# Kernel tuning notes

Measured on AMD Instinct MI355X. Metric: run time of the kernel, lower is better.

Reference implementation:

```python
import jax, jax.numpy as jnp
import numpy as np

N, E = 50000, 800000
IN, HID, OUT = 256, 128, 128


def setup_inputs() -> dict:
    key = jax.random.key(0)
    ks = jax.random.split(key, 6)
    x = jax.random.normal(ks[0], (N, IN), dtype=jnp.float32)
    edge_index = jax.random.randint(ks[1], (2, E), 0, N, dtype=jnp.int32)
    # xavier_normal-ish scales (exact init values irrelevant for correctness baseline)
    W1 = jax.random.normal(ks[2], (IN, HID), dtype=jnp.float32) * (1.414 / np.sqrt(IN))
    att_src = jax.random.normal(ks[3], (HID,), dtype=jnp.float32) * 0.1
    att_dst = jax.random.normal(ks[4], (HID,), dtype=jnp.float32) * 0.1
    W2 = jax.random.normal(ks[5], (HID, OUT), dtype=jnp.float32) * (1.414 / np.sqrt(HID))
    return {"x": x, "edge_index": edge_index, "W1": W1,
            "att_src": att_src, "att_dst": att_dst, "W2": W2}


def _gat_layer(x, edge_index, W, a_src, a_dst):
    """GATConv(heads=1, concat=False, add_self_loops=False, dropout=0), attention=True."""
    n = x.shape[0]
    src, dst = edge_index[0], edge_index[1]  # message x_j = h[src], grouped by index = dst
    h = x @ W                                 # (N, C)
    e_src = h @ a_src                         # (N,) per-node attention logits
    e_dst = h @ a_dst                         # (N,)
    # per-edge: sigmoid(alpha_j + alpha_i), then scatter-softmax over dst neighborhoods
    alpha = jax.nn.sigmoid(e_src[src] + e_dst[dst])             # (E,)
    m = jax.ops.segment_max(alpha, dst, num_segments=n)          # stable softmax max
    ex = jnp.exp(alpha - m[dst])
    denom = jax.ops.segment_sum(ex, dst, num_segments=n)
    w = ex / denom[dst]                                          # (E,)
    # scatter-add aggregation of weighted source features; heads=1 so mean over heads is identity
    return jax.ops.segment_sum(h[src] * w[:, None], dst, num_segments=n)  # (N, C)


def reference(x, edge_index, W1, att_src, att_dst, W2):
    h1 = jax.nn.elu(_gat_layer(x, edge_index, W1, att_src, att_dst))
    # conv2 called with attention=False: mm(h1, W2).view(N,1,C).mean(1) == plain linear
    return h1 @ W2
```

## Files before the change

kernel.cpp:

```cpp
#include <hip/hip_runtime.h>
#include <hip/hip_bf16.h>

#define N_NODES 50000
#define N_EDGES 800000
#define DIN 256
#define DHID 128
#define DOUT 128
#define NBUCK 196
#define BINBLK 256
#define EPB 3125
#define BINIT 13

typedef __attribute__((ext_vector_type(8))) short bf16x8;
typedef __attribute__((ext_vector_type(4))) float f32x4;

__device__ inline unsigned short f2b(float f) {
    __hip_bfloat16 b = __float2bfloat16(f);
    return *reinterpret_cast<unsigned short*>(&b);
}

__global__ __launch_bounds__(256) void convW_kernel(
    const float* __restrict__ W1, const float* __restrict__ W2,
    unsigned short* __restrict__ W1t, unsigned short* __restrict__ W2t)
{
    int i = blockIdx.x * 256 + threadIdx.x;
    if (i < DIN * DHID) {
        int n = i >> 8, k = i & 255;
        W1t[i] = f2b(W1[k * DHID + n]);
    } else {
        int j = i - DIN * DHID;
        int n = j >> 7, k = j & 127;
        W2t[j] = f2b(W2[k * DOUT + n]);
    }
}

__global__ __launch_bounds__(256) void gemm1_mfma(
    const float* __restrict__ x,
    const unsigned short* __restrict__ W1t,
    const float* __restrict__ att_src,
    const float* __restrict__ att_dst,
    unsigned short* __restrict__ hb,
    float* __restrict__ es,
    float* __restrict__ ed)
{
    __shared__ unsigned short W1s[DHID * DIN];

    const int tid = threadIdx.x;
    const int wave = tid >> 6, lane = tid & 63;
    const int row0 = blockIdx.x * 64 + wave * 16;
    const int m = lane & 15, q = lane >> 4;

    {
        const float4* src = (const float4*)W1t;
        float4* dst = (float4*)W1s;
        #pragma unroll
        for (int i = 0; i < 16; ++i)
            dst[tid + i * 256] = src[tid + i * 256];
    }
    __syncthreads();

    int r  = row0 + m;
    int rc = (r < N_NODES) ? r : 0;

    f32x4 acc[8];
    #pragma unroll
    for (int t = 0; t < 8; ++t) acc[t] = (f32x4){0.f, 0.f, 0.f, 0.f};

    const float* xr = x + (size_t)rc * DIN + q * 8;
    const short* wp = (const short*)W1s + q * 8;

    #pragma unroll
    for (int kt = 0; kt < 8; ++kt) {
        float4 f0 = *(const float4*)(xr + kt * 32);
        float4 f1 = *(const float4*)(xr + kt * 32 + 4);
        bf16x8 a;
        a[0] = (short)f2b(f0.x); a[1] = (short)f2b(f0.y);
        a[2] = (short)f2b(f0.z); a[3] = (short)f2b(f0.w);
        a[4] = (short)f2b(f1.x); a[5] = (short)f2b(f1.y);
        a[6] = (short)f2b(f1.z); a[7] = (short)f2b(f1.w);
        #pragma unroll
        for (int t = 0; t < 8; ++t) {
            bf16x8 b = *(const bf16x8*)(wp + (t * 16 + m) * DIN + kt * 32);
            acc[t] = __builtin_amdgcn_mfma_f32_16x16x32_bf16(a, b, acc[t], 0, 0, 0);
        }
    }

    #pragma unroll
    for (int reg = 0; reg < 4; ++reg) {
        int rr = row0 + q * 4 + reg;
        if (rr < N_NODES) {
            #pragma unroll
            for (int t = 0; t < 8; ++t)
                hb[(size_t)rr * DHID + t * 16 + m] = f2b(acc[t][reg]);
        }
    }

    float esr[4] = {0.f, 0.f, 0.f, 0.f}, edr[4] = {0.f, 0.f, 0.f, 0.f};
    #pragma unroll
    for (int t = 0; t < 8; ++t) {
        float as = att_src[t * 16 + m];
        float ad = att_dst[t * 16 + m];
        #pragma unroll
        for (int reg = 0; reg < 4; ++reg) {
            esr[reg] += acc[t][reg] * as;
            edr[reg] += acc[t][reg] * ad;
        }
    }
    #pragma unroll
    for (int off = 8; off; off >>= 1)
        #pragma unroll
        for (int reg = 0; reg < 4; ++reg) {
            esr[reg] += __shfl_xor(esr[reg], off);
            edr[reg] += __shfl_xor(edr[reg], off);
        }
    if (m == 0) {
        #pragma unroll
        for (int reg = 0; reg < 4; ++reg) {
            int rr = row0 + q * 4 + reg;
            if (rr < N_NODES) { es[rr] = esr[reg]; ed[rr] = edr[reg]; }
        }
    }
}

__global__ __launch_bounds__(256) void lhist_kernel(
    const int* __restrict__ ei, int* __restrict__ blockHist,
    int* __restrict__ bucketTotals)
{
    __shared__ int h[NBUCK];
    const int t = threadIdx.x, blk = blockIdx.x;
    if (t < NBUCK) h[t] = 0;
    __syncthreads();
    const int base = blk * EPB;
    #pragma unroll 1
    for (int it = 0; it < BINIT; ++it) {
        int e = base + it * 256 + t;
        if (e < base + EPB)
            atomicAdd(&h[ei[N_EDGES + e] >> 8], 1);
    }
    __syncthreads();
    if (t < NBUCK) {
        blockHist[t * 256 + blk] = h[t];
        atomicAdd(&bucketTotals[t], h[t]);
    }
}

__global__ __launch_bounds__(256) void scanfused_kernel(
    const int* __restrict__ bucketTotals,
    const int* __restrict__ blockHist,
    int* __restrict__ matrixScan)
{
    __shared__ int bs[256];
    __shared__ int s[256];
    const int t = threadIdx.x, b = blockIdx.x;

    bs[t] = (t < NBUCK) ? bucketTotals[t] : 0;
    __syncthreads();
    #pragma unroll
    for (int off = 1; off < 256; off <<= 1) {
        int u = (t >= off) ? bs[t - off] : 0;
        __syncthreads();
        bs[t] += u;
        __syncthreads();
    }
    const int base = (b == 0) ? 0 : bs[b - 1];

    int c = blockHist[b * 256 + t];
    s[t] = c;
    __syncthreads();
    #pragma unroll
    for (int off = 1; off < 256; off <<= 1) {
        int u = (t >= off) ? s[t - off] : 0;
        __syncthreads();
        s[t] += u;
        __syncthreads();
    }
    matrixScan[b * 256 + t] = base + s[t] - c;
}

__global__ __launch_bounds__(256) void binpass_kernel(
    const int* __restrict__ ei,
    const float* __restrict__ es,
    const float* __restrict__ ed,
    const int* __restrict__ matrixScan,
    int2* __restrict__ binned)
{
    __shared__ int lcur[NBUCK];
    const int t = threadIdx.x, blk = blockIdx.x;
    if (t < NBUCK) lcur[t] = matrixScan[t * 256 + blk];
    __syncthreads();
    const int base = blk * EPB;
    #pragma unroll 1
    for (int it = 0; it < BINIT; ++it) {
        int e = base + it * 256 + t;
        if (e < base + EPB) {
            int s = ei[e];
            int d = ei[N_EDGES + e];
            float a  = es[s] + ed[d];
            float sg = 1.f / (1.f + __expf(-a));
            float w  = __expf(sg);
            int pos = atomicAdd(&lcur[d >> 8], 1);
            binned[pos] = make_int2(s | ((d & 255) << 16), __float_as_int(w));
        }
    }
}

__global__ __launch_bounds__(256) void sortpass_kernel(
    const int2* __restrict__ binned,
    const int* __restrict__ matrixScan,
    int2* __restrict__ sortedSW,
    int* __restrict__ offset,
    int* __restrict__ count)
{
    __shared__ int lhist[256], lscan[256], lcur[256];
    const int t = threadIdx.x, b = blockIdx.x;
    const int start = matrixScan[b * 256];
    const int end   = (b == NBUCK - 1) ? N_EDGES : matrixScan[(b + 1) * 256];
    const int cnt   = end - start;

    lhist[t] = 0;
    __syncthreads();
    for (int i = t; i < cnt; i += 256)
        atomicAdd(&lhist[(binned[start + i].x >> 16) & 255], 1);
    __syncthreads();

    int v = lhist[t];
    lscan[t] = v;
    __syncthreads();
    #pragma unroll
    for (int off = 1; off < 256; off <<= 1) {
        int u = (t >= off) ? lscan[t - off] : 0;
        __syncthreads();
        lscan[t] += u;
        __syncthreads();
    }
    int excl = lscan[t] - v;

    int node = (b << 8) + t;
    if (node < N_NODES) { offset[node] = start + excl; count[node] = v; }
    lcur[t] = excl;
    __syncthreads();

    for (int i = t; i < cnt; i += 256) {
        int2 ent = binned[start + i];
        int dlow = (ent.x >> 16) & 255;
        int pos = atomicAdd(&lcur[dlow], 1);
        sortedSW[start + pos] = make_int2(ent.x & 0xFFFF, ent.y);
    }
}

__global__ __launch_bounds__(256) void agg_kernel(
    const int2* __restrict__ sortedSW,
    const int* __restrict__ offset,
    const int* __restrict__ count,
    const unsigned short* __restrict__ hb,
    unsigned int* __restrict__ h1b)
{
    int node = (blockIdx.x * 256 + threadIdx.x) >> 6;
    int lane = threadIdx.x & 63;
    if (node >= N_NODES) return;

    int beg = offset[node];
    int deg = count[node];

    float2 acc = make_float2(0.f, 0.f);
    float wsum = 0.f;

    for (int base = 0; base < deg; base += 64) {
        int cnt = min(64, deg - base);
        int2 sw = (lane < cnt) ? sortedSW[beg + base + lane] : make_int2(0, 0);
        int j = 0;

#define TIER(T)                                                                 \
        for (; j + T <= cnt; j += T) {                                          \
            unsigned uu[T]; float ww[T];                                        \
            _Pragma("unroll")                                                   \
            for (int k = 0; k < T; ++k) {                                       \
                int s_ = __builtin_amdgcn_readlane(sw.x, j + k);                \
                uu[k] = *(const unsigned*)(hb + (size_t)s_ * DHID + 2 * lane);  \
            }                                                                   \
            _Pragma("unroll")                                                   \
            for (int k = 0; k < T; ++k)                                         \
                ww[k] = __uint_as_float(                                        \
                    (unsigned)__builtin_amdgcn_readlane(sw.y, j + k));          \
            _Pragma("unroll")                                                   \
            for (int k = 0; k < T; ++k) {                                       \
                wsum  += ww[k];                                                 \
                acc.x += ww[k] * __uint_as_float(uu[k] << 16);                  \
                acc.y += ww[k] * __uint_as_float(uu[k] & 0xffff0000u);          \
            }                                                                   \
        }

        TIER(16)
        TIER(8)
        TIER(4)
#undef TIER
        for (; j < cnt; ++j) {
            int   sj = __builtin_amdgcn_readlane(sw.x, j);
            float wj = __uint_as_float((unsigned)__builtin_amdgcn_readlane(sw.y, j));
            unsigned u = *(const unsigned*)(hb + (size_t)sj * DHID + 2 * lane);
            acc.x += wj * __uint_as_float(u << 16);
            acc.y += wj * __uint_as_float(u & 0xffff0000u);
            wsum  += wj;
        }
    }
    float inv = (deg > 0) ? 1.f / wsum : 0.f;
    float v0 = acc.x * inv, v1 = acc.y * inv;
    float e0 = v0 > 0.f ? v0 : (__expf(v0) - 1.f);
    float e1 = v1 > 0.f ? v1 : (__expf(v1) - 1.f);
    h1b[(size_t)node * (DHID / 2) + lane] =
        (unsigned)f2b(e0) | ((unsigned)f2b(e1) << 16);
}

__global__ __launch_bounds__(256) void gemm2_mfma(
    const unsigned short* __restrict__ h1b,
    const unsigned short* __restrict__ W2t,
    float* __restrict__ out)
{
    __shared__ unsigned short W2s[DOUT * DHID];

    const int tid = threadIdx.x;
    const int wave = tid >> 6, lane = tid & 63;
    const int row0 = blockIdx.x * 64 + wave * 16;
    const int m = lane & 15, q = lane >> 4;

    {
        const float4* src = (const float4*)W2t;
        float4* dst = (float4*)W2s;
        #pragma unroll
        for (int i = 0; i < 8; ++i)
            dst[tid + i * 256] = src[tid + i * 256];
    }
    __syncthreads();

    int r  = row0 + m;
    int rc = (r < N_NODES) ? r : 0;

    f32x4 acc[8];
    #pragma unroll
    for (int t = 0; t < 8; ++t) acc[t] = (f32x4){0.f, 0.f, 0.f, 0.f};

    const short* xp = (const short*)h1b + (size_t)rc * DHID + q * 8;
    const short* wp = (const short*)W2s + q * 8;

    #pragma unroll
    for (int kt = 0; kt < 4; ++kt) {
        bf16x8 a = *(const bf16x8*)(xp + kt * 32);
        #pragma unroll
        for (int t = 0; t < 8; ++t) {
            bf16x8 b = *(const bf16x8*)(wp + (t * 16 + m) * DHID + kt * 32);
            acc[t] = __builtin_amdgcn_mfma_f32_16x16x32_bf16(a, b, acc[t], 0, 0, 0);
        }
    }

    #pragma unroll
    for (int reg = 0; reg < 4; ++reg) {
        int rr = row0 + q * 4 + reg;
        if (rr < N_NODES) {
            #pragma unroll
            for (int t = 0; t < 8; ++t)
                out[(size_t)rr * DOUT + t * 16 + m] = acc[t][reg];
        }
    }
}

extern "C" void kernel_launch(void* const* d_in, const int* in_sizes, int n_in,
                              void* d_out, int out_size, void* d_ws, size_t ws_size,
                              hipStream_t stream)
{
    const float* x    = (const float*)d_in[0];
    const int*   ei   = (const int*)d_in[1];
    const float* W1   = (const float*)d_in[2];
    const float* asrc = (const float*)d_in[3];
    const float* adst = (const float*)d_in[4];
    const float* W2   = (const float*)d_in[5];
    float*       out  = (float*)d_out;

    char* p = (char*)d_ws;
    unsigned short* hb  = (unsigned short*)p;  p += (size_t)N_NODES * DHID * 2;
    unsigned int*   h1b = (unsigned int*)p;    p += (size_t)N_NODES * DHID * 2;
    unsigned short* W1t = (unsigned short*)p;  p += (size_t)DHID * DIN * 2;
    unsigned short* W2t = (unsigned short*)p;  p += (size_t)DOUT * DHID * 2;
    float* es     = (float*)p;  p += (size_t)N_NODES * 4;
    float* ed     = (float*)p;  p += (size_t)N_NODES * 4;
    int*   offset = (int*)p;    p += (size_t)N_NODES * 4;
    int*   count  = (int*)p;    p += (size_t)N_NODES * 4;
    int*   blockHist    = (int*)p; p += (size_t)NBUCK * 256 * 4;
    int*   matrixScan   = (int*)p; p += (size_t)NBUCK * 256 * 4;
    int*   bucketTotals = (int*)p; p += 256 * 4;
    int2*  binned   = (int2*)p; p += (size_t)N_EDGES * 8;
    int2*  sortedSW = (int2*)p; p += (size_t)N_EDGES * 8;

    hipMemsetAsync(bucketTotals, 0, NBUCK * sizeof(int), stream);

    convW_kernel<<<(DIN * DHID + DHID * DOUT) / 256, 256, 0, stream>>>(W1, W2, W1t, W2t);

    gemm1_mfma<<<(N_NODES + 63) / 64, 256, 0, stream>>>(x, W1t, asrc, adst, hb, es, ed);

    lhist_kernel    <<<BINBLK, 256, 0, stream>>>(ei, blockHist, bucketTotals);
    scanfused_kernel<<<NBUCK, 256, 0, stream>>>(bucketTotals, blockHist, matrixScan);
    binpass_kernel  <<<BINBLK, 256, 0, stream>>>(ei, es, ed, matrixScan, binned);
    sortpass_kernel <<<NBUCK, 256, 0, stream>>>(binned, matrixScan, sortedSW, offset, count);

    agg_kernel<<<(N_NODES * 64 + 255) / 256, 256, 0, stream>>>(
        sortedSW, offset, count, hb, h1b);

    gemm2_mfma<<<(N_NODES + 63) / 64, 256, 0, stream>>>((const unsigned short*)h1b, W2t, out);
}
```

Before: 195.2 us.

## Switch GEMMs to single-wave 32x32x16 MFMA blocks reading weights from global

Both dense GEMMs now use one-wave blocks of 32 rows with the 32x32x16 bf16 MFMA instead of four-wave blocks of 64 rows with 16x16x32 MFMA. The shared-memory staging of the transposed weight matrix and its barrier are removed, so B fragments are loaded straight from global memory and rely on L2/L1 caching. This is meant to cut the per-block LDS fill cost (64KB for W1) and raise occupancy, at the cost of more blocks and repeated global weight reads.

```diff
diff --git a/kernel.cpp b/kernel.cpp
--- a/kernel.cpp
+++ b/kernel.cpp
@@ -12,7 +12,7 @@
 #define BINIT 13
 
 typedef __attribute__((ext_vector_type(8))) short bf16x8;
-typedef __attribute__((ext_vector_type(4))) float f32x4;
+typedef __attribute__((ext_vector_type(16))) float f32x16;
 
 __device__ inline unsigned short f2b(float f) {
     __hip_bfloat16 b = __float2bfloat16(f);
@@ -34,7 +34,7 @@
     }
 }
 
-__global__ __launch_bounds__(256) void gemm1_mfma(
+__global__ __launch_bounds__(64) void gemm1_mfma(
     const float* __restrict__ x,
     const unsigned short* __restrict__ W1t,
     const float* __restrict__ att_src,
@@ -43,81 +43,74 @@
     float* __restrict__ es,
     float* __restrict__ ed)
 {
-    __shared__ unsigned short W1s[DHID * DIN];
-
-    const int tid = threadIdx.x;
-    const int wave = tid >> 6, lane = tid & 63;
-    const int row0 = blockIdx.x * 64 + wave * 16;
-    const int m = lane & 15, q = lane >> 4;
-
-    {
-        const float4* src = (const float4*)W1t;
-        float4* dst = (float4*)W1s;
-        #pragma unroll
-        for (int i = 0; i < 16; ++i)
-            dst[tid + i * 256] = src[tid + i * 256];
-    }
-    __syncthreads();
-
-    int r  = row0 + m;
+    const int lane = threadIdx.x;
+    const int row0 = blockIdx.x * 32;
+    const int c  = lane & 31;
+    const int hf = lane >> 5;
+
+    int r  = row0 + c;
     int rc = (r < N_NODES) ? r : 0;
 
-    f32x4 acc[8];
-    #pragma unroll
-    for (int t = 0; t < 8; ++t) acc[t] = (f32x4){0.f, 0.f, 0.f, 0.f};
-
-    const float* xr = x + (size_t)rc * DIN + q * 8;
-    const short* wp = (const short*)W1s + q * 8;
-
-    #pragma unroll
-    for (int kt = 0; kt < 8; ++kt) {
-        float4 f0 = *(const float4*)(xr + kt * 32);
-        float4 f1 = *(const float4*)(xr + kt * 32 + 4);
+    f32x16 acc[4];
+    #pragma unroll
+    for (int t = 0; t < 4; ++t)
+        #pragma unroll
+        for (int g = 0; g < 16; ++g) acc[t][g] = 0.f;
+
+    const float* xr = x + (size_t)rc * DIN + hf * 8;
+    const unsigned short* wb = W1t + hf * 8;
+
+    #pragma unroll
+    for (int kt = 0; kt < 16; ++kt) {
+        float4 f0 = *(const float4*)(xr + kt * 16);
+        float4 f1 = *(const float4*)(xr + kt * 16 + 4);
         bf16x8 a;
         a[0] = (short)f2b(f0.x); a[1] = (short)f2b(f0.y);
         a[2] = (short)f2b(f0.z); a[3] = (short)f2b(f0.w);
         a[4] = (short)f2b(f1.x); a[5] = (short)f2b(f1.y);
         a[6] = (short)f2b(f1.z); a[7] = (short)f2b(f1.w);
         #pragma unroll
-        for (int t = 0; t < 8; ++t) {
-            bf16x8 b = *(const bf16x8*)(wp + (t * 16 + m) * DIN + kt * 32);
-            acc[t] = __builtin_amdgcn_mfma_f32_16x16x32_bf16(a, b, acc[t], 0, 0, 0);
-        }
-    }
-
-    #pragma unroll
-    for (int reg = 0; reg < 4; ++reg) {
-        int rr = row0 + q * 4 + reg;
-        if (rr < N_NODES) {
+        for (int t = 0; t < 4; ++t) {
+            bf16x8 b = *(const bf16x8*)(wb + (size_t)(t * 32 + c) * DIN + kt * 16);
+            acc[t] = __builtin_amdgcn_mfma_f32_32x32x16_bf16(a, b, acc[t], 0, 0, 0);
+        }
+    }
+
+    #pragma unroll
+    for (int reg = 0; reg < 16; ++reg) {
+        int row = row0 + (reg & 3) + 4 * hf + 8 * (reg >> 2);
+        if (row < N_NODES) {
             #pragma unroll
-            for (int t = 0; t < 8; ++t)
-                hb[(size_t)rr * DHID + t * 16 + m] = f2b(acc[t][reg]);
-        }
-    }
-
-    float esr[4] = {0.f, 0.f, 0.f, 0.f}, edr[4] = {0.f, 0.f, 0.f, 0.f};
-    #pragma unroll
-    for (int t = 0; t < 8; ++t) {
-        float as = att_src[t * 16 + m];
-        float ad = att_dst[t * 16 + m];
-        #pragma unroll
-        for (int reg = 0; reg < 4; ++reg) {
+            for (int t = 0; t < 4; ++t)
+                hb[(size_t)row * DHID + t * 32 + c] = f2b(acc[t][reg]);
+        }
+    }
+
+    float esr[16], edr[16];
+    #pragma unroll
+    for (int reg = 0; reg < 16; ++reg) { esr[reg] = 0.f; edr[reg] = 0.f; }
+    #pragma unroll
+    for (int t = 0; t < 4; ++t) {
+        float as = att_src[t * 32 + c];
+        float ad = att_dst[t * 32 + c];
+        #pragma unroll
+        for (int reg = 0; reg < 16; ++reg) {
             esr[reg] += acc[t][reg] * as;
             edr[reg] += acc[t][reg] * ad;
         }
     }
     #pragma unroll
-    for (int off = 8; off; off >>= 1)
-        #pragma unroll
-        for (int reg = 0; reg < 4; ++reg) {
+    for (int off = 16; off; off >>= 1)
+        #pragma unroll
+        for (int reg = 0; reg < 16; ++reg) {
             esr[reg] += __shfl_xor(esr[reg], off);
             edr[reg] += __shfl_xor(edr[reg], off);
         }
-    if (m == 0) {
-        #pragma unroll
-        for (int reg = 0; reg < 4; ++reg) {
-            int rr = row0 + q * 4 + reg;
-            if (rr < N_NODES) { es[rr] = esr[reg]; ed[rr] = edr[reg]; }
+    if (c == 0) {
+        #pragma unroll
+        for (int reg = 0; reg < 16; ++reg) {
+            int row = row0 + (reg & 3) + 4 * hf + 8 * (reg >> 2);
+            if (row < N_NODES) { es[row] = esr[reg]; ed[row] = edr[reg]; }
         }
     }
 }
@@ -311,54 +304,45 @@
         (unsigned)f2b(e0) | ((unsigned)f2b(e1) << 16);
 }
 
-__global__ __launch_bounds__(256) void gemm2_mfma(
+__global__ __launch_bounds__(64) void gemm2_mfma(
     const unsigned short* __restrict__ h1b,
     const unsigned short* __restrict__ W2t,
     float* __restrict__ out)
 {
-    __shared__ unsigned short W2s[DOUT * DHID];
-
-    const int tid = threadIdx.x;
-    const int wave = tid >> 6, lane = tid & 63;
-    const int row0 = blockIdx.x * 64 + wave * 16;
-    const int m = lane & 15, q = lane >> 4;
-
-    {
-        const float4* src = (const float4*)W2t;
-        float4* dst = (float4*)W2s;
-        #pragma unroll
-        for (int i = 0; i < 8; ++i)
-            dst[tid + i * 256] = src[tid + i * 256];
-    }
-    __syncthreads();
-
-    int r  = row0 + m;
+    const int lane = threadIdx.x;
+    const int row0 = blockIdx.x * 32;
+    const int c  = lane & 31;
+    const int hf = lane >> 5;
+
+    int r  = row0 + c;
     int rc = (r < N_NODES) ? r : 0;
 
-    f32x4 acc[8];
-    #pragma unroll
-    for (int t = 0; t < 8; ++t) acc[t] = (f32x4){0.f, 0.f, 0.f, 0.f};
-
-    const short* xp = (const short*)h1b + (size_t)rc * DHID + q * 8;
-    const short* wp = (const short*)W2s + q * 8;
-
-    #pragma unroll
-    for (int kt = 0; kt < 4; ++kt) {
-        bf16x8 a = *(const bf16x8*)(xp + kt * 32);
-        #pragma unroll
-        for (int t = 0; t < 8; ++t) {
-            bf16x8 b = *(const bf16x8*)(wp + (t * 16 + m) * DHID + kt * 32);
-            acc[t] = __builtin_amdgcn_mfma_f32_16x16x32_bf16(a, b, acc[t], 0, 0, 0);
-        }
-    }
-
-    #pragma unroll
-    for (int reg = 0; reg < 4; ++reg) {
-        int rr = row0 + q * 4 + reg;
-        if (rr < N_NODES) {
+    f32x16 acc[4];
+    #pragma unroll
+    for (int t = 0; t < 4; ++t)
+        #pragma unroll
+        for (int g = 0; g < 16; ++g) acc[t][g] = 0.f;
+
+    const unsigned short* ar = h1b + (size_t)rc * DHID + hf * 8;
+    const unsigned short* wb = W2t + hf * 8;
+
+    #pragma unroll
+    for (int kt = 0; kt < 8; ++kt) {
+        bf16x8 a = *(const bf16x8*)(ar + kt * 16);
+        #pragma unroll
+        for (int t = 0; t < 4; ++t) {
+            bf16x8 b = *(const bf16x8*)(wb + (size_t)(t * 32 + c) * DHID + kt * 16);
+            acc[t] = __builtin_amdgcn_mfma_f32_32x32x16_bf16(a, b, acc[t], 0, 0, 0);
+        }
+    }
+
+    #pragma unroll
+    for (int reg = 0; reg < 16; ++reg) {
+        int row = row0 + (reg & 3) + 4 * hf + 8 * (reg >> 2);
+        if (row < N_NODES) {
             #pragma unroll
-            for (int t = 0; t < 8; ++t)
-                out[(size_t)rr * DOUT + t * 16 + m] = acc[t][reg];
+            for (int t = 0; t < 4; ++t)
+                out[(size_t)row * DOUT + t * 32 + c] = acc[t][reg];
         }
     }
 }
@@ -394,7 +378,7 @@
 
     convW_kernel<<<(DIN * DHID + DHID * DOUT) / 256, 256, 0, stream>>>(W1, W2, W1t, W2t);
 
-    gemm1_mfma<<<(N_NODES + 63) / 64, 256, 0, stream>>>(x, W1t, asrc, adst, hb, es, ed);
+    gemm1_mfma<<<(N_NODES + 31) / 32, 64, 0, stream>>>(x, W1t, asrc, adst, hb, es, ed);
 
     lhist_kernel    <<<BINBLK, 256, 0, stream>>>(ei, blockHist, bucketTotals);
     scanfused_kernel<<<NBUCK, 256, 0, stream>>>(bucketTotals, blockHist, matrixScan);
@@ -404,5 +388,6 @@
     agg_kernel<<<(N_NODES * 64 + 255) / 256, 256, 0, stream>>>(
         sortedSW, offset, count, hb, h1b);
 
-    gemm2_mfma<<<(N_NODES + 63) / 64, 256, 0, stream>>>((const unsigned short*)h1b, W2t, out);
-}
+    gemm2_mfma<<<(N_NODES + 31) / 32, 64, 0, stream>>>(
+        (const unsigned short*)h1b, W2t, out);
+}
```

Result: slower. 209.5 us (+7.4%).
